# Performance work log

Measured on AMD Instinct MI355X. Metric: run time of the kernel, lower is better.

Reference implementation:

```python
import jax, jax.numpy as jnp
import numpy as np

N, D = 32768, 1024

def setup_inputs() -> dict:
    key = jax.random.key(0)
    k1, k2, k3 = jax.random.split(key, 3)
    elg = jax.random.normal(k1, (N, D), dtype=jnp.float32)
    eth = jax.random.normal(k2, (N, D), dtype=jnp.float32)
    weight = jax.random.normal(k3, (D, D), dtype=jnp.float32)
    return {"elg": elg, "eth": eth, "weight": weight}

def reference(elg, eth, weight):
    # out[n] = elg[n] @ W @ eth[n]  -- batched bilinear form, fully fused
    return jnp.einsum('nd,de,ne->n', elg, weight, eth)
```

## Files before the change

### kernel.cpp

```cpp
#include <hip/hip_runtime.h>
#include <hip/hip_bf16.h>

typedef __attribute__((ext_vector_type(8))) short short8;
typedef __attribute__((ext_vector_type(4))) float float4v;
typedef __attribute__((ext_vector_type(4))) unsigned int uint4v;

#define DDIM 1024
#define ETH_STRIDE 40

__device__ __forceinline__ unsigned short f2bf(float f) {
  unsigned u = __builtin_bit_cast(unsigned, f);
  unsigned r = (u + 0x7fffu + ((u >> 16) & 1u)) >> 16;
  return (unsigned short)r;
}
__device__ __forceinline__ unsigned pk2(float lo, float hi) {
  return (unsigned)f2bf(lo) | ((unsigned)f2bf(hi) << 16);
}
__device__ __forceinline__ void cvt8(const float* src, unsigned short* dst) {
  float4v a = *(const float4v*)(src);
  float4v b = *(const float4v*)(src + 4);
  uint4v pk;
  pk.x = pk2(a.x, a.y); pk.y = pk2(a.z, a.w);
  pk.z = pk2(b.x, b.y); pk.w = pk2(b.z, b.w);
  *(uint4v*)dst = pk;
}

__global__ __launch_bounds__(256) void convert_all(const float* __restrict__ W,
                                                   const float* __restrict__ eth,
                                                   unsigned short* __restrict__ Wb,
                                                   unsigned short* __restrict__ ethB) {
  int b = blockIdx.x;
  if (b < 512) {
    size_t i = ((size_t)b * 256 + threadIdx.x) * 8;
    cvt8(W + i, Wb + i);
  } else {
    size_t i = ((size_t)(b - 512) * 256 + threadIdx.x) * 8;
    cvt8(eth + i, ethB + i);
  }
}
__global__ __launch_bounds__(256) void convert_w(const float* __restrict__ W,
                                                 unsigned short* __restrict__ Wb) {
  size_t i = ((size_t)blockIdx.x * 256 + threadIdx.x) * 8;
  cvt8(W + i, Wb + i);
}

__global__ __launch_bounds__(256, 3) void bilinear_bf16(const float* __restrict__ elg,
                                                        const unsigned short* __restrict__ ethB,
                                                        const unsigned short* __restrict__ Wb,
                                                        float* __restrict__ out) {
  __shared__ unsigned short Wbuf[2][256 * 32];
  __shared__ unsigned short ethL[2][64 * 32];
  __shared__ float wsum[4][64];

  const int tid  = threadIdx.x;
  const int lane = tid & 63;
  const int w    = tid >> 6;
  const int quad = lane >> 4;
  const int l15  = lane & 15;
  const int m0   = (blockIdx.x >> 2) * 64;
  const int d0   = (blockIdx.x & 3) * 256;
  const int wr = lane >> 2, wu = lane & 3;

  auto stage = [&](int ek, int buf) {
    const int e0 = ek * 32;
#pragma unroll
    for (int j = 0; j < 4; ++j) {
      int r  = (w * 4 + j) * 16 + wr;
      int ug = wu ^ ((r >> 1) & 3);
      const unsigned short* gp = Wb + (size_t)(d0 + r) * DDIM + e0 + ug * 8;
      unsigned short* lp = &Wbuf[buf][(w * 4 + j) * 512 + lane * 8];
      __builtin_amdgcn_global_load_lds(
          (const __attribute__((address_space(1))) unsigned int*)gp,
          (__attribute__((address_space(3))) unsigned int*)lp, 16, 0, 0);
    }
    {
      int er = w * 16 + wr;
      const unsigned short* gp = ethB + (size_t)(m0 + er) * DDIM + e0 + wu * 8;
      unsigned short* lp = &ethL[buf][w * 512 + lane * 8];
      __builtin_amdgcn_global_load_lds(
          (const __attribute__((address_space(1))) unsigned int*)gp,
          (__attribute__((address_space(3))) unsigned int*)lp, 16, 0, 0);
    }
  };

  float4v acc[4][4];
#pragma unroll
  for (int ct = 0; ct < 4; ++ct)
#pragma unroll
    for (int rt = 0; rt < 4; ++rt)
      acc[ct][rt] = (float4v){0.f, 0.f, 0.f, 0.f};

  stage(0, 0);
  __syncthreads();

  for (int ek = 0; ek < 32; ++ek) {
    const int cur = ek & 1;
    if (ek < 31) stage(ek + 1, cur ^ 1);

    short8 aF[4], bF[4];
#pragma unroll
    for (int rt = 0; rt < 4; ++rt)
      aF[rt] = *(const short8*)&ethL[cur][(rt * 16 + l15) * 32 + quad * 8];
#pragma unroll
    for (int ct = 0; ct < 4; ++ct) {
      int dl = w * 64 + ct * 16 + l15;
      int pu = quad ^ ((dl >> 1) & 3);
      bF[ct] = *(const short8*)&Wbuf[cur][dl * 32 + pu * 8];
    }
#pragma unroll
    for (int ct = 0; ct < 4; ++ct)
#pragma unroll
      for (int rt = 0; rt < 4; ++rt)
        acc[ct][rt] = __builtin_amdgcn_mfma_f32_16x16x32_bf16(aF[rt], bF[ct], acc[ct][rt], 0, 0, 0);

    __syncthreads();
  }

  float p[16];
#pragma unroll
  for (int j = 0; j < 16; ++j) p[j] = 0.f;
#pragma unroll
  for (int ct = 0; ct < 4; ++ct) {
    int col = d0 + w * 64 + ct * 16 + l15;
#pragma unroll
    for (int rt = 0; rt < 4; ++rt) {
      const float* ep = elg + (size_t)(m0 + rt * 16 + quad * 4) * DDIM + col;
#pragma unroll
      for (int i = 0; i < 4; ++i)
        p[rt * 4 + i] += acc[ct][rt][i] * ep[(size_t)i * DDIM];
    }
  }
#pragma unroll
  for (int off = 1; off < 16; off <<= 1)
#pragma unroll
    for (int j = 0; j < 16; ++j)
      p[j] += __shfl_xor(p[j], off);
  if (l15 == 0) {
#pragma unroll
    for (int rt = 0; rt < 4; ++rt)
#pragma unroll
      for (int i = 0; i < 4; ++i)
        wsum[w][rt * 16 + quad * 4 + i] = p[rt * 4 + i];
  }
  __syncthreads();
  if (tid < 64) {
    float s = wsum[0][tid] + wsum[1][tid] + wsum[2][tid] + wsum[3][tid];
    atomicAdd(&out[m0 + tid], s);
  }
}

__global__ __launch_bounds__(256, 3) void bilinear_fp32eth(const float* __restrict__ elg,
                                                           const float* __restrict__ eth,
                                                           const unsigned short* __restrict__ Wb,
                                                           float* __restrict__ out) {
  __shared__ unsigned short ethL[64 * ETH_STRIDE];
  __shared__ unsigned short Wbuf[256 * 32];
  __shared__ float wsum[4][64];
  const int tid  = threadIdx.x;
  const int lane = tid & 63;
  const int w    = tid >> 6;
  const int quad = lane >> 4;
  const int l15  = lane & 15;
  const int m0   = (blockIdx.x >> 2) * 64;
  const int d0   = (blockIdx.x & 3) * 256;
  const int erow = tid >> 2, eunit = tid & 3;
  const float* esrc = eth + (size_t)(m0 + erow) * DDIM + eunit * 8;
  const int wr = lane >> 2, wu = lane & 3;
  float4v er0 = *(const float4v*)(esrc);
  float4v er1 = *(const float4v*)(esrc + 4);
  float4v acc[4][4];
#pragma unroll
  for (int ct = 0; ct < 4; ++ct)
#pragma unroll
    for (int rt = 0; rt < 4; ++rt)
      acc[ct][rt] = (float4v){0.f, 0.f, 0.f, 0.f};
  for (int ek = 0; ek < 32; ++ek) {
    const int e0 = ek * 32;
    __syncthreads();
    {
      uint4v pk;
      pk.x = pk2(er0.x, er0.y); pk.y = pk2(er0.z, er0.w);
      pk.z = pk2(er1.x, er1.y); pk.w = pk2(er1.z, er1.w);
      *(uint4v*)&ethL[erow * ETH_STRIDE + eunit * 8] = pk;
    }
#pragma unroll
    for (int j = 0; j < 4; ++j) {
      int r  = (w * 4 + j) * 16 + wr;
      int ug = wu ^ ((r >> 1) & 3);
      const unsigned short* gp = Wb + (size_t)(d0 + r) * DDIM + e0 + ug * 8;
      unsigned short* lp = &Wbuf[(w * 4 + j) * 512 + lane * 8];
      __builtin_amdgcn_global_load_lds(
          (const __attribute__((address_space(1))) unsigned int*)gp,
          (__attribute__((address_space(3))) unsigned int*)lp, 16, 0, 0);
    }
    __syncthreads();
    short8 aF[4], bF[4];
#pragma unroll
    for (int rt = 0; rt < 4; ++rt)
      aF[rt] = *(const short8*)&ethL[(rt * 16 + l15) * ETH_STRIDE + quad * 8];
#pragma unroll
    for (int ct = 0; ct < 4; ++ct) {
      int dl = w * 64 + ct * 16 + l15;
      int pu = quad ^ ((dl >> 1) & 3);
      bF[ct] = *(const short8*)&Wbuf[dl * 32 + pu * 8];
    }
    if (ek < 31) {
      const float* s = esrc + (e0 + 32);
      er0 = *(const float4v*)(s);
      er1 = *(const float4v*)(s + 4);
    }
#pragma unroll
    for (int ct = 0; ct < 4; ++ct)
#pragma unroll
      for (int rt = 0; rt < 4; ++rt)
        acc[ct][rt] = __builtin_amdgcn_mfma_f32_16x16x32_bf16(aF[rt], bF[ct], acc[ct][rt], 0, 0, 0);
  }
  float p[16];
#pragma unroll
  for (int j = 0; j < 16; ++j) p[j] = 0.f;
#pragma unroll
  for (int ct = 0; ct < 4; ++ct) {
    int col = d0 + w * 64 + ct * 16 + l15;
#pragma unroll
    for (int rt = 0; rt < 4; ++rt) {
      const float* ep = elg + (size_t)(m0 + rt * 16 + quad * 4) * DDIM + col;
#pragma unroll
      for (int i = 0; i < 4; ++i)
        p[rt * 4 + i] += acc[ct][rt][i] * ep[(size_t)i * DDIM];
    }
  }
#pragma unroll
  for (int off = 1; off < 16; off <<= 1)
#pragma unroll
    for (int j = 0; j < 16; ++j)
      p[j] += __shfl_xor(p[j], off);
  if (l15 == 0) {
#pragma unroll
    for (int rt = 0; rt < 4; ++rt)
#pragma unroll
      for (int i = 0; i < 4; ++i)
        wsum[w][rt * 16 + quad * 4 + i] = p[rt * 4 + i];
  }
  __syncthreads();
  if (tid < 64) {
    float s = wsum[0][tid] + wsum[1][tid] + wsum[2][tid] + wsum[3][tid];
    atomicAdd(&out[m0 + tid], s);
  }
}

extern "C" void kernel_launch(void* const* d_in, const int* in_sizes, int n_in,
                              void* d_out, int out_size, void* d_ws, size_t ws_size,
                              hipStream_t stream) {
  (void)in_sizes; (void)n_in;
  const float* elg = (const float*)d_in[0];
  const float* eth = (const float*)d_in[1];
  const float* W   = (const float*)d_in[2];
  float* out = (float*)d_out;
  unsigned short* Wb   = (unsigned short*)d_ws;
  unsigned short* ethB = (unsigned short*)((char*)d_ws + (2 << 20));

  const size_t need = (2ull << 20) + (64ull << 20);
  hipMemsetAsync(d_out, 0, (size_t)out_size * sizeof(float), stream);
  if (ws_size >= need) {
    convert_all<<<dim3(512 + 16384), dim3(256), 0, stream>>>(W, eth, Wb, ethB);
    bilinear_bf16<<<dim3(2048), dim3(256), 0, stream>>>(elg, ethB, Wb, out);
  } else {
    convert_w<<<dim3(512), dim3(256), 0, stream>>>(W, Wb);
    bilinear_fp32eth<<<dim3(2048), dim3(256), 0, stream>>>(elg, eth, Wb, out);
  }
}
```

Before: 365.6 us.

## Retile bf16 bilinear kernel to square 128x128 block tiles with 2x2 warp grid

Changes the per-block tile in the bf16 kernel from 64 rows by 256 weight columns to 128 rows by 128 columns, with the four warps arranged 2x2 so each computes a 64x64 sub-tile. Eth staging now also uses the XOR swizzle. Per k-step the block loads fewer bytes per MFMA, which improves arithmetic intensity and cuts redundant W and eth traffic from L2. Shared memory per block drops, and launch bounds are raised to 4 blocks per CU for occupancy. Each block now issues more atomic adds, and the grid has the same number of blocks, so tail behaviour may change.

```diff
diff --git a/kernel.cpp b/kernel.cpp
--- a/kernel.cpp
+++ b/kernel.cpp
@@ -6,7 +6,6 @@
 typedef __attribute__((ext_vector_type(4))) unsigned int uint4v;
 
 #define DDIM 1024
-#define ETH_STRIDE 40
 
 __device__ __forceinline__ unsigned short f2bf(float f) {
   unsigned u = __builtin_bit_cast(unsigned, f);
@@ -44,12 +43,12 @@
   cvt8(W + i, Wb + i);
 }
 
-__global__ __launch_bounds__(256, 3) void bilinear_bf16(const float* __restrict__ elg,
+__global__ __launch_bounds__(256, 4) void bilinear_bf16(const float* __restrict__ elg,
                                                         const unsigned short* __restrict__ ethB,
                                                         const unsigned short* __restrict__ Wb,
                                                         float* __restrict__ out) {
-  __shared__ unsigned short Wbuf[2][256 * 32];
-  __shared__ unsigned short ethL[2][64 * 32];
+  __shared__ unsigned short Wbuf[2][128 * 32];
+  __shared__ unsigned short ethL[2][128 * 32];
   __shared__ float wsum[4][64];
 
   const int tid  = threadIdx.x;
@@ -57,29 +56,29 @@
   const int w    = tid >> 6;
   const int quad = lane >> 4;
   const int l15  = lane & 15;
-  const int m0   = (blockIdx.x >> 2) * 64;
-  const int d0   = (blockIdx.x & 3) * 256;
+  const int rowhalf = w >> 1;
+  const int colhalf = w & 1;
+  const int m0   = (blockIdx.x >> 3) * 128;
+  const int d0   = (blockIdx.x & 7) * 128;
   const int wr = lane >> 2, wu = lane & 3;
 
   auto stage = [&](int ek, int buf) {
     const int e0 = ek * 32;
 #pragma unroll
-    for (int j = 0; j < 4; ++j) {
-      int r  = (w * 4 + j) * 16 + wr;
-      int ug = wu ^ ((r >> 1) & 3);
-      const unsigned short* gp = Wb + (size_t)(d0 + r) * DDIM + e0 + ug * 8;
-      unsigned short* lp = &Wbuf[buf][(w * 4 + j) * 512 + lane * 8];
+    for (int j = 0; j < 2; ++j) {
+      const int R0 = w * 16 + j * 64;
+      const int r  = R0 + wr;
+      const int ug = wu ^ ((r >> 1) & 3);
+      const unsigned short* gw = Wb   + (size_t)(d0 + r) * DDIM + e0 + ug * 8;
+      const unsigned short* ge = ethB + (size_t)(m0 + r) * DDIM + e0 + ug * 8;
+      unsigned short* lw = &Wbuf[buf][R0 * 32 + lane * 8];
+      unsigned short* le = &ethL[buf][R0 * 32 + lane * 8];
       __builtin_amdgcn_global_load_lds(
-          (const __attribute__((address_space(1))) unsigned int*)gp,
-          (__attribute__((address_space(3))) unsigned int*)lp, 16, 0, 0);
-    }
-    {
-      int er = w * 16 + wr;
-      const unsigned short* gp = ethB + (size_t)(m0 + er) * DDIM + e0 + wu * 8;
-      unsigned short* lp = &ethL[buf][w * 512 + lane * 8];
+          (const __attribute__((address_space(1))) unsigned int*)gw,
+          (__attribute__((address_space(3))) unsigned int*)lw, 16, 0, 0);
       __builtin_amdgcn_global_load_lds(
-          (const __attribute__((address_space(1))) unsigned int*)gp,
-          (__attribute__((address_space(3))) unsigned int*)lp, 16, 0, 0);
+          (const __attribute__((address_space(1))) unsigned int*)ge,
+          (__attribute__((address_space(3))) unsigned int*)le, 16, 0, 0);
     }
   };
 
@@ -99,13 +98,16 @@
 
     short8 aF[4], bF[4];
 #pragma unroll
-    for (int rt = 0; rt < 4; ++rt)
-      aF[rt] = *(const short8*)&ethL[cur][(rt * 16 + l15) * 32 + quad * 8];
+    for (int rt = 0; rt < 4; ++rt) {
+      int r  = rowhalf * 64 + rt * 16 + l15;
+      int pu = quad ^ ((r >> 1) & 3);
+      aF[rt] = *(const short8*)&ethL[cur][r * 32 + pu * 8];
+    }
 #pragma unroll
     for (int ct = 0; ct < 4; ++ct) {
-      int dl = w * 64 + ct * 16 + l15;
-      int pu = quad ^ ((dl >> 1) & 3);
-      bF[ct] = *(const short8*)&Wbuf[cur][dl * 32 + pu * 8];
+      int r  = colhalf * 64 + ct * 16 + l15;
+      int pu = quad ^ ((r >> 1) & 3);
+      bF[ct] = *(const short8*)&Wbuf[cur][r * 32 + pu * 8];
     }
 #pragma unroll
     for (int ct = 0; ct < 4; ++ct)
@@ -121,10 +123,10 @@
   for (int j = 0; j < 16; ++j) p[j] = 0.f;
 #pragma unroll
   for (int ct = 0; ct < 4; ++ct) {
-    int col = d0 + w * 64 + ct * 16 + l15;
+    int col = d0 + colhalf * 64 + ct * 16 + l15;
 #pragma unroll
     for (int rt = 0; rt < 4; ++rt) {
-      const float* ep = elg + (size_t)(m0 + rt * 16 + quad * 4) * DDIM + col;
+      const float* ep = elg + (size_t)(m0 + rowhalf * 64 + rt * 16 + quad * 4) * DDIM + col;
 #pragma unroll
       for (int i = 0; i < 4; ++i)
         p[rt * 4 + i] += acc[ct][rt][i] * ep[(size_t)i * DDIM];
@@ -143,12 +145,14 @@
         wsum[w][rt * 16 + quad * 4 + i] = p[rt * 4 + i];
   }
   __syncthreads();
-  if (tid < 64) {
-    float s = wsum[0][tid] + wsum[1][tid] + wsum[2][tid] + wsum[3][tid];
+  if (tid < 128) {
+    int local = tid & 63, half = tid >> 6;
+    float s = wsum[half * 2][local] + wsum[half * 2 + 1][local];
     atomicAdd(&out[m0 + tid], s);
   }
 }
 
+#define ETH_STRIDE 40
 __global__ __launch_bounds__(256, 3) void bilinear_fp32eth(const float* __restrict__ elg,
                                                            const float* __restrict__ eth,
                                                            const unsigned short* __restrict__ Wb,
```

Measured after the change: 354.8 us. 1.03x faster.
